# Kernel tuning notes

Measured on AMD Instinct MI355X. Metric: run time of the kernel, lower is better.

The kernel has to match this reference:

```python
import jax, jax.numpy as jnp
import numpy as np

BS, SEQ, C, NC, H, W = 8, 512, 512, 5, 768, 768


def setup_inputs() -> dict:
    key = jax.random.key(0)
    k1, k2, k3, k4, k5, k6, k7, k8 = jax.random.split(key, 8)
    fuse_embeddings = jax.random.normal(k1, (BS, SEQ, C), dtype=jnp.float32)
    class_labels = jax.random.normal(k2, (BS, NC, H, W), dtype=jnp.float32)
    # valid boxes: x0<x1<=W, y0<y1<=H (coords order: x0, y0, x1, y1)
    x0 = jax.random.randint(k3, (BS, SEQ), 0, W - 1)
    y0 = jax.random.randint(k4, (BS, SEQ), 0, H - 1)
    x1 = jnp.minimum(x0 + jax.random.randint(k5, (BS, SEQ), 1, 64), W)
    y1 = jnp.minimum(y0 + jax.random.randint(k6, (BS, SEQ), 1, 16), H)
    coords = jnp.stack([x0, y0, x1, y1], axis=-1).astype(jnp.int32)
    mask = jax.random.randint(k7, (BS, SEQ), 0, 2).astype(jnp.int32)
    # classification_net (Linear) params
    bound = 1.0 / np.sqrt(C)
    Wc = jax.random.uniform(k8, (NC, C), minval=-bound, maxval=bound, dtype=jnp.float32)
    bc = jnp.zeros((NC,), dtype=jnp.float32)
    return {"fuse_embeddings": fuse_embeddings, "class_labels": class_labels,
            "Wc": Wc, "bc": bc, "coords": coords, "mask": mask}


def _forward(fuse_embeddings, class_labels, Wc, bc, coords, mask):
    bs, seq_len, _ = fuse_embeddings.shape
    nc = Wc.shape[0]
    # linear classifier over all tokens: [bs, seq, nc]
    logits = jnp.einsum("bsc,nc->bsn", fuse_embeddings, Wc) + bc
    # per-pixel hard label: [bs, H, W]
    lab = jnp.argmax(class_labels, axis=1)
    onehot = jax.nn.one_hot(lab, nc, dtype=logits.dtype)  # [bs, H, W, nc]
    # padded integral image -> O(1) box histograms (replaces per-ROI bincount)
    ii = jnp.cumsum(jnp.cumsum(onehot, axis=1), axis=2)
    ii = jnp.pad(ii, ((0, 0), (1, 0), (1, 0), (0, 0)))  # [bs, H+1, W+1, nc]
    x0, y0, x1, y1 = coords[..., 0], coords[..., 1], coords[..., 2], coords[..., 3]
    # degenerate-box fix from the original code
    y1 = jnp.where(y1 == y0, y1 + 1, y1)
    x1 = jnp.where(x1 == x0, x1 + 1, x1)
    b_idx = jnp.arange(bs)[:, None]
    g = lambda y, x: ii[b_idx, y, x, :]
    counts = g(y1, x1) - g(y0, x1) - g(y1, x0) + g(y0, x0)  # [bs, seq, nc]
    maj = jnp.argmax(counts, axis=-1)  # majority-vote label, first-max tiebreak like bincount().argmax()
    # masked-mean cross entropy (CE over tokens with mask==1)
    logp = jax.nn.log_softmax(logits, axis=-1)
    nll = -jnp.take_along_axis(logp, maj[..., None], axis=-1)[..., 0]
    m = (mask == 1).astype(logits.dtype)
    return jnp.sum(nll * m) / jnp.sum(m)


def reference(fuse_embeddings, class_labels, Wc, bc, coords, mask):
    return _forward(fuse_embeddings, class_labels, Wc, bc, coords, mask)
```

## Files before the change

kernel.cpp:

```cpp
#include <hip/hip_runtime.h>

#define BS 8
#define SEQ 512
#define CDIM 512
#define NC 5
#define IMG_H 768
#define IMG_W 768
#define HW (IMG_H * IMG_W)
#define NTOK (BS * SEQ)
#define NBLK (NTOK / 4)

__global__ __launch_bounds__(256) void token_kernel(
    const float* __restrict__ emb,
    const float* __restrict__ cls,
    const float* __restrict__ Wc,
    const float* __restrict__ bc,
    const int*   __restrict__ coords,
    const int*   __restrict__ mask,
    float2* __restrict__ ws)
{
    const int t     = threadIdx.x;
    const int wave  = t >> 6;
    const int lane  = t & 63;
    const int b     = blockIdx.x & 7;
    const int slot  = blockIdx.x >> 3;
    const int token = (b << 9) + slot * 4 + wave;

    int x0 = coords[token * 4 + 0];
    int y0 = coords[token * 4 + 1];
    int x1 = coords[token * 4 + 2];
    int y1 = coords[token * 4 + 3];
    if (y1 == y0) y1++;
    if (x1 == x0) x1++;
    if (x1 > IMG_W) x1 = IMG_W;
    if (y1 > IMG_H) y1 = IMG_H;

    unsigned long long hp = 0ull;
    {
        const int xx = x0 + lane;
        const bool xok = (xx < x1);
        const float* p0 = cls + (size_t)b * NC * HW + y0 * IMG_W + xx;
#pragma unroll 4
        for (int yy = y0; yy < y1; ++yy, p0 += IMG_W) {
            if (xok) {
                const float v0 = p0[0 * HW];
                const float v1 = p0[1 * HW];
                const float v2 = p0[2 * HW];
                const float v3 = p0[3 * HW];
                const float v4 = p0[4 * HW];
                int lab = 0; float best = v0;
                if (v1 > best) { best = v1; lab = 1; }
                if (v2 > best) { best = v2; lab = 2; }
                if (v3 > best) { best = v3; lab = 3; }
                if (v4 > best) { best = v4; lab = 4; }
                hp += 1ull << (lab * 12);
            }
        }
    }

    const float* e = emb + (size_t)token * CDIM + lane * 8;
    const float4 e0 = *(const float4*)(e);
    const float4 e1 = *(const float4*)(e + 4);
    float part[NC];
#pragma unroll
    for (int c = 0; c < NC; ++c) {
        const float* w = Wc + c * CDIM + lane * 8;
        const float4 w0 = *(const float4*)(w);
        const float4 w1 = *(const float4*)(w + 4);
        part[c] = e0.x * w0.x + e0.y * w0.y + e0.z * w0.z + e0.w * w0.w
                + e1.x * w1.x + e1.y * w1.y + e1.z * w1.z + e1.w * w1.w;
    }

#pragma unroll
    for (int off = 32; off >= 1; off >>= 1) {
#pragma unroll
        for (int c = 0; c < NC; ++c) part[c] += __shfl_down(part[c], off);
        hp += __shfl_down(hp, off);
    }

    __shared__ float2 s_pair[4];
    if (lane == 0) {
        float l[NC];
#pragma unroll
        for (int c = 0; c < NC; ++c) l[c] = part[c] + bc[c];

        int maj = 0;
        int bestc = (int)(hp & 4095);
#pragma unroll
        for (int c = 1; c < NC; ++c) {
            const int hc = (int)((hp >> (12 * c)) & 4095);
            if (hc > bestc) { bestc = hc; maj = c; }
        }

        float m = l[0];
#pragma unroll
        for (int c = 1; c < NC; ++c) m = fmaxf(m, l[c]);
        float s = 0.0f;
#pragma unroll
        for (int c = 0; c < NC; ++c) s += __expf(l[c] - m);
        const float nll = m + __logf(s) - l[maj];

        const float mk = (mask[token] == 1) ? 1.0f : 0.0f;
        s_pair[wave] = make_float2(nll * mk, mk);
    }
    __syncthreads();

    if (t == 0) {
        const float2 a = s_pair[0], b2 = s_pair[1],
                     c2 = s_pair[2], d2 = s_pair[3];
        ws[blockIdx.x] = make_float2(a.x + b2.x + c2.x + d2.x,
                                     a.y + b2.y + c2.y + d2.y);
    }
}

__global__ __launch_bounds__(256) void finalize_kernel(
    const float2* __restrict__ ws, float* __restrict__ out)
{
    float a = 0.0f, bsum = 0.0f;
#pragma unroll
    for (int i = threadIdx.x; i < NBLK; i += 256) {
        const float2 v = ws[i];
        a += v.x; bsum += v.y;
    }
#pragma unroll
    for (int off = 32; off >= 1; off >>= 1) {
        a    += __shfl_down(a, off);
        bsum += __shfl_down(bsum, off);
    }
    __shared__ float sa[4], sb[4];
    const int wave = threadIdx.x >> 6;
    if ((threadIdx.x & 63) == 0) { sa[wave] = a; sb[wave] = bsum; }
    __syncthreads();
    if (threadIdx.x == 0) {
        a    = sa[0] + sa[1] + sa[2] + sa[3];
        bsum = sb[0] + sb[1] + sb[2] + sb[3];
        out[0] = a / bsum;
    }
}

extern "C" void kernel_launch(void* const* d_in, const int* in_sizes, int n_in,
                              void* d_out, int out_size, void* d_ws, size_t ws_size,
                              hipStream_t stream) {
    const float* emb    = (const float*)d_in[0];
    const float* cls    = (const float*)d_in[1];
    const float* Wc     = (const float*)d_in[2];
    const float* bc     = (const float*)d_in[3];
    const int*   coords = (const int*)d_in[4];
    const int*   mask   = (const int*)d_in[5];
    float* out = (float*)d_out;
    float2* ws = (float2*)d_ws;

    token_kernel<<<NBLK, 256, 0, stream>>>(emb, cls, Wc, bc, coords, mask, ws);
    finalize_kernel<<<1, 256, 0, stream>>>(ws, out);
}
```

Measured before the change: 146.3 us.

## Assign one token per 128-thread block, splitting box rows across two waves

```diff
diff --git a/kernel.cpp b/kernel.cpp
--- a/kernel.cpp
+++ b/kernel.cpp
@@ -8,9 +8,8 @@
 #define IMG_W 768
 #define HW (IMG_H * IMG_W)
 #define NTOK (BS * SEQ)
-#define NBLK (NTOK / 4)
 
-__global__ __launch_bounds__(256) void token_kernel(
+__global__ __launch_bounds__(128) void token_kernel(
     const float* __restrict__ emb,
     const float* __restrict__ cls,
     const float* __restrict__ Wc,
@@ -23,8 +22,7 @@
     const int wave  = t >> 6;
     const int lane  = t & 63;
     const int b     = blockIdx.x & 7;
-    const int slot  = blockIdx.x >> 3;
-    const int token = (b << 9) + slot * 4 + wave;
+    const int token = (b << 9) + (blockIdx.x >> 3);
 
     int x0 = coords[token * 4 + 0];
     int y0 = coords[token * 4 + 1];
@@ -39,9 +37,9 @@
     {
         const int xx = x0 + lane;
         const bool xok = (xx < x1);
-        const float* p0 = cls + (size_t)b * NC * HW + y0 * IMG_W + xx;
+        const float* p0 = cls + (size_t)b * NC * HW + (y0 + wave) * IMG_W + xx;
 #pragma unroll 4
-        for (int yy = y0; yy < y1; ++yy, p0 += IMG_W) {
+        for (int yy = y0 + wave; yy < y1; yy += 2, p0 += 2 * IMG_W) {
             if (xok) {
                 const float v0 = p0[0 * HW];
                 const float v1 = p0[1 * HW];
@@ -58,17 +56,12 @@
         }
     }
 
-    const float* e = emb + (size_t)token * CDIM + lane * 8;
-    const float4 e0 = *(const float4*)(e);
-    const float4 e1 = *(const float4*)(e + 4);
+    const float4 e0 = *(const float4*)(emb + (size_t)token * CDIM + t * 4);
     float part[NC];
 #pragma unroll
     for (int c = 0; c < NC; ++c) {
-        const float* w = Wc + c * CDIM + lane * 8;
-        const float4 w0 = *(const float4*)(w);
-        const float4 w1 = *(const float4*)(w + 4);
-        part[c] = e0.x * w0.x + e0.y * w0.y + e0.z * w0.z + e0.w * w0.w
-                + e1.x * w1.x + e1.y * w1.y + e1.z * w1.z + e1.w * w1.w;
+        const float4 w0 = *(const float4*)(Wc + c * CDIM + t * 4);
+        part[c] = e0.x * w0.x + e0.y * w0.y + e0.z * w0.z + e0.w * w0.w;
     }
 
 #pragma unroll
@@ -78,17 +71,27 @@
         hp += __shfl_down(hp, off);
     }
 
-    __shared__ float2 s_pair[4];
+    __shared__ float              s_part[2][NC];
+    __shared__ unsigned long long s_hp[2];
     if (lane == 0) {
+#pragma unroll
+        for (int c = 0; c < NC; ++c) s_part[wave][c] = part[c];
+        s_hp[wave] = hp;
+    }
+    __syncthreads();
+
+    if (t == 0) {
+        const unsigned long long h = s_hp[0] + s_hp[1];
         float l[NC];
 #pragma unroll
-        for (int c = 0; c < NC; ++c) l[c] = part[c] + bc[c];
+        for (int c = 0; c < NC; ++c)
+            l[c] = s_part[0][c] + s_part[1][c] + bc[c];
 
         int maj = 0;
-        int bestc = (int)(hp & 4095);
+        int bestc = (int)(h & 4095);
 #pragma unroll
         for (int c = 1; c < NC; ++c) {
-            const int hc = (int)((hp >> (12 * c)) & 4095);
+            const int hc = (int)((h >> (12 * c)) & 4095);
             if (hc > bestc) { bestc = hc; maj = c; }
         }
 
@@ -101,15 +104,7 @@
         const float nll = m + __logf(s) - l[maj];
 
         const float mk = (mask[token] == 1) ? 1.0f : 0.0f;
-        s_pair[wave] = make_float2(nll * mk, mk);
-    }
-    __syncthreads();
-
-    if (t == 0) {
-        const float2 a = s_pair[0], b2 = s_pair[1],
-                     c2 = s_pair[2], d2 = s_pair[3];
-        ws[blockIdx.x] = make_float2(a.x + b2.x + c2.x + d2.x,
-                                     a.y + b2.y + c2.y + d2.y);
+        ws[blockIdx.x] = make_float2(nll * mk, mk);
     }
 }
 
@@ -118,7 +113,7 @@
 {
     float a = 0.0f, bsum = 0.0f;
 #pragma unroll
-    for (int i = threadIdx.x; i < NBLK; i += 256) {
+    for (int i = threadIdx.x; i < NTOK; i += 256) {
         const float2 v = ws[i];
         a += v.x; bsum += v.y;
     }
@@ -150,6 +145,6 @@
     float* out = (float*)d_out;
     float2* ws = (float2*)d_ws;
 
-    token_kernel<<<NBLK, 256, 0, stream>>>(emb, cls, Wc, bc, coords, mask, ws);
+    token_kernel<<<NTOK, 128, 0, stream>>>(emb, cls, Wc, bc, coords, mask, ws);
     finalize_kernel<<<1, 256, 0, stream>>>(ws, out);
 }
```

Measured after the change: 150.9 us. 3.2% more time.
